# Optimization experiments

Measured on AMD Instinct MI355X. Metric: run time of the kernel, lower is better.

## Reference

```python
import jax, jax.numpy as jnp
import numpy as np

D_MODEL = 1024
NUM_HEADS = 16
D_K = D_MODEL // NUM_HEADS


def setup_inputs() -> dict:
    key = jax.random.key(0)
    ks = jax.random.split(key, 11)
    B, S = 4, 2048
    s = 1.0 / np.sqrt(D_MODEL)
    return {
        "query": jax.random.normal(ks[0], (B, S, D_MODEL), jnp.float32),
        "key": jax.random.normal(ks[1], (B, S, D_MODEL), jnp.float32),
        "value": jax.random.normal(ks[2], (B, S, D_MODEL), jnp.float32),
        "Wq": jax.random.normal(ks[3], (D_MODEL, D_MODEL), jnp.float32) * s,
        "bq": jnp.zeros((D_MODEL,), jnp.float32),
        "Wk": jax.random.normal(ks[4], (D_MODEL, D_MODEL), jnp.float32) * s,
        "bk": jnp.zeros((D_MODEL,), jnp.float32),
        "Wv": jax.random.normal(ks[5], (D_MODEL, D_MODEL), jnp.float32) * s,
        "bv": jnp.zeros((D_MODEL,), jnp.float32),
        "Wo": jax.random.normal(ks[6], (D_MODEL, D_MODEL), jnp.float32) * s,
        "bo": jnp.zeros((D_MODEL,), jnp.float32),
    }


def reference(query, key, value, Wq, bq, Wk, bk, Wv, bv, Wo, bo):
    B, Sq, _ = query.shape
    Sk = key.shape[1]
    # linear projections (torch Linear: x @ W.T + b)
    q = query @ Wq.T + bq
    k = key @ Wk.T + bk
    v = value @ Wv.T + bv
    # [B, H, S, d_k]
    q = q.reshape(B, Sq, NUM_HEADS, D_K).transpose(0, 2, 1, 3)
    k = k.reshape(B, Sk, NUM_HEADS, D_K).transpose(0, 2, 1, 3)
    v = v.reshape(B, Sk, NUM_HEADS, D_K).transpose(0, 2, 1, 3)
    scores = jnp.einsum("bhqd,bhkd->bhqk", q, k) / jnp.sqrt(jnp.float32(D_K)).astype(q.dtype)
    attn = jax.nn.softmax(scores, axis=-1)
    out = jnp.einsum("bhqk,bhkd->bhqd", attn, v)
    out = out.transpose(0, 2, 1, 3).reshape(B, Sq, D_MODEL)
    return out @ Wo.T + bo
```

## Files before the change

### kernel.cpp

```cpp
#include <hip/hip_runtime.h>
#include <hip/hip_bf16.h>
#include <cstdint>
#include <cstddef>

typedef __attribute__((ext_vector_type(8))) short bf16x8;
typedef __attribute__((ext_vector_type(4))) short bf16x4;
typedef __attribute__((ext_vector_type(4))) float f32x4;
typedef __attribute__((ext_vector_type(2))) unsigned int u32x2;

#define NH 16
#define DK 64
#define SEQ 2048
#define DM 1024
#define QSCALE 0.18033688011112042f

__device__ __forceinline__ short f2bf(float f) {
    union { float f; unsigned u; } x; x.f = f;
    unsigned r = x.u + 0x7fffu + ((x.u >> 16) & 1u);
    return (short)(r >> 16);
}

__device__ __forceinline__ unsigned pk2(float a, float b) {
    union { float f; unsigned u; } x, y; x.f = a; y.f = b;
    return __builtin_amdgcn_perm(y.u + 0x8000u, x.u + 0x8000u, 0x07060302u);
}

__device__ __forceinline__ void glds16(const short* g, short* l) {
    __builtin_amdgcn_global_load_lds((const __attribute__((address_space(1))) unsigned int*)g,
                                     (__attribute__((address_space(3))) unsigned int*)l, 16, 0, 0);
}

__global__ __launch_bounds__(256)
void cvt_x(const float* __restrict__ src, short* __restrict__ dst)
{
    int i = (blockIdx.x * 256 + threadIdx.x) * 8;
    float4 a = *(const float4*)&src[i];
    float4 b = *(const float4*)&src[i + 4];
    bf16x8 o = { f2bf(a.x), f2bf(a.y), f2bf(a.z), f2bf(a.w),
                 f2bf(b.x), f2bf(b.y), f2bf(b.z), f2bf(b.w) };
    *(bf16x8*)&dst[i] = o;
}

__global__ __launch_bounds__(256)
void cvt_w(const float* __restrict__ Wq, const float* __restrict__ Wk,
           const float* __restrict__ Wv, const float* __restrict__ Wo,
           short* __restrict__ dst)
{
    int z = blockIdx.y;
    const float* s = (z == 0) ? Wq : (z == 1) ? Wk : (z == 2) ? Wv : Wo;
    float sc = (z == 0) ? QSCALE : 1.0f;
    int i = (blockIdx.x * 256 + threadIdx.x) * 8;
    float4 a = *(const float4*)&s[i];
    float4 b = *(const float4*)&s[i + 4];
    bf16x8 o = { f2bf(a.x * sc), f2bf(a.y * sc), f2bf(a.z * sc), f2bf(a.w * sc),
                 f2bf(b.x * sc), f2bf(b.y * sc), f2bf(b.z * sc), f2bf(b.w * sc) };
    *(bf16x8*)&dst[(size_t)z * DM * DM + i] = o;
}

#define GEMM_CORE(P0, OFF0, P1, OFF1)                                                      \
    __shared__ short As[128 * 32];                                                         \
    __shared__ short Bs[128 * 32];                                                         \
    f32x4 acc[4][4] = {};                                                                  \
    const int t = threadIdx.x;                                                             \
    const int lane = t & 63;                                                               \
    const int w = t >> 6;                                                                  \
    const int wm = (w >> 1) * 64, wn = (w & 1) * 64;                                       \
    const int l15 = lane & 15, quad = lane >> 4;                                           \
    const int g0 = t, g1 = 256 + t;                                                        \
    const int r0 = g0 >> 2, r1 = g1 >> 2;                                                  \
    const int c0 = ((g0 & 3) ^ ((r0 >> 1) & 3)) * 8;                                       \
    const int c1 = ((g1 & 3) ^ ((r1 >> 1) & 3)) * 8;                                       \
    for (int k0 = 0; k0 < DM; k0 += 32) {                                                  \
        glds16(&P0[(size_t)(OFF0 + r0) * DM + k0 + c0], &As[g0 * 8]);                      \
        glds16(&P0[(size_t)(OFF0 + r1) * DM + k0 + c1], &As[g1 * 8]);                      \
        glds16(&P1[(size_t)(OFF1 + r0) * DM + k0 + c0], &Bs[g0 * 8]);                      \
        glds16(&P1[(size_t)(OFF1 + r1) * DM + k0 + c1], &Bs[g1 * 8]);                      \
        __syncthreads();                                                                   \
        bf16x8 a[4], b[4];                                                                 \
        _Pragma("unroll")                                                                  \
        for (int i = 0; i < 4; i++) {                                                      \
            int row = wm + i * 16 + l15;                                                   \
            a[i] = *(bf16x8*)&As[row * 32 + (quad ^ ((row >> 1) & 3)) * 8];                \
        }                                                                                  \
        _Pragma("unroll")                                                                  \
        for (int j = 0; j < 4; j++) {                                                      \
            int row = wn + j * 16 + l15;                                                   \
            b[j] = *(bf16x8*)&Bs[row * 32 + (quad ^ ((row >> 1) & 3)) * 8];                \
        }                                                                                  \
        _Pragma("unroll")                                                                  \
        for (int i = 0; i < 4; i++)                                                        \
            _Pragma("unroll")                                                              \
            for (int j = 0; j < 4; j++)                                                    \
                acc[i][j] = __builtin_amdgcn_mfma_f32_16x16x32_bf16(a[i], b[j], acc[i][j], 0, 0, 0); \
        __syncthreads();                                                                   \
    }

__global__ __launch_bounds__(256)
void gemm_qk(const short* __restrict__ X, const short* __restrict__ W,
             const float* __restrict__ bias, short* __restrict__ dst, float bscale)
{
    const int tn = blockIdx.x * 128;
    const int tm = blockIdx.y * 128;
    GEMM_CORE(W, tn, X, tm)

#pragma unroll
    for (int i = 0; i < 4; i++) {
        int n0 = tn + wm + i * 16 + quad * 4;
        float4 b4 = *(const float4*)&bias[n0];
        int h = n0 >> 6, d0 = n0 & 63;
#pragma unroll
        for (int j = 0; j < 4; j++) {
            int m = tm + wn + j * 16 + l15;
            int bb = m >> 11, s = m & (SEQ - 1);
            u32x2 u = { pk2(acc[i][j][0] + b4.x * bscale, acc[i][j][1] + b4.y * bscale),
                        pk2(acc[i][j][2] + b4.z * bscale, acc[i][j][3] + b4.w * bscale) };
            *(u32x2*)&dst[((((size_t)(bb * NH + h)) * SEQ + s) << 6) + d0] = u;
        }
    }
}

__global__ __launch_bounds__(256)
void gemm_v(const short* __restrict__ X, const short* __restrict__ W,
            const float* __restrict__ bias, short* __restrict__ dst)
{
    const int tn = blockIdx.x * 128;
    const int tm = blockIdx.y * 128;
    GEMM_CORE(X, tm, W, tn)

#pragma unroll
    for (int j = 0; j < 4; j++) {
        int n = tn + wn + j * 16 + l15;
        float bn = bias[n];
        int h = n >> 6, d = n & 63;
#pragma unroll
        for (int i = 0; i < 4; i++) {
            int m0 = tm + wm + i * 16 + quad * 4;
            int bb = m0 >> 11, s0 = m0 & (SEQ - 1);
            u32x2 u = { pk2(acc[i][j][0] + bn, acc[i][j][1] + bn),
                        pk2(acc[i][j][2] + bn, acc[i][j][3] + bn) };
            *(u32x2*)&dst[((size_t)((bb * NH + h) * 64 + d)) * SEQ + s0] = u;
        }
    }
}

__global__ __launch_bounds__(256)
void out_proj(const short* __restrict__ A, const short* __restrict__ W,
              const float* __restrict__ bias, float* __restrict__ out)
{
    const int tn = blockIdx.x * 128;
    const int tm = blockIdx.y * 128;
    GEMM_CORE(A, tm, W, tn)

#pragma unroll
    for (int j = 0; j < 4; j++) {
        int n = tn + wn + j * 16 + l15;
        float bn = bias[n];
#pragma unroll
        for (int i = 0; i < 4; i++)
#pragma unroll
            for (int r = 0; r < 4; r++) {
                int m = tm + wm + i * 16 + quad * 4 + r;
                out[(size_t)m * DM + n] = acc[i][j][r] + bn;
            }
    }
}

__global__ __launch_bounds__(256, 4)
void attn(const short* __restrict__ Q, const short* __restrict__ K, const short* __restrict__ V,
          short* __restrict__ O)
{
    const int bh = blockIdx.x;
    const int b = bh >> 4, h = bh & 15;
    const int qt = blockIdx.y;
    const size_t base = (size_t)bh * SEQ * DK;
    const size_t vbase = (size_t)bh * DK * SEQ;

    const int t = threadIdx.x;
    const int lane = t & 63;
    const int w = t >> 6;
    const int l15 = lane & 15, quad = lane >> 4;
    const int l7 = l15 & 7;

    __shared__ short Kt[64 * 64];
    __shared__ short Vt[64 * 64];
    __shared__ short Pt[4][32 * 64];

    bf16x8 qb[2][2];
    const int qrow0 = qt * 128 + w * 32;
#pragma unroll
    for (int nq = 0; nq < 2; nq++)
#pragma unroll
        for (int kd = 0; kd < 2; kd++)
            qb[nq][kd] = *(const bf16x8*)&Q[base + (size_t)(qrow0 + nq * 16 + l15) * DK + kd * 32 + quad * 8];

    f32x4 oT[4][2] = {};
    float l_[2] = { 0.0f, 0.0f };

    const int sr = t >> 2;
    const int sc = (t & 3) * 16;
    const int sg0 = (((t & 3) * 2) ^ (sr & 7)) * 8;
    const int sg1 = (((t & 3) * 2 + 1) ^ (sr & 7)) * 8;

    bf16x8 kr0 = *(const bf16x8*)&K[base + (size_t)sr * DK + sc];
    bf16x8 kr1 = *(const bf16x8*)&K[base + (size_t)sr * DK + sc + 8];
    bf16x8 vr0 = *(const bf16x8*)&V[vbase + (size_t)sr * SEQ + sc];
    bf16x8 vr1 = *(const bf16x8*)&V[vbase + (size_t)sr * SEQ + sc + 8];

    for (int kt = 0; kt < SEQ / 64; kt++) {
        *(bf16x8*)&Kt[sr * 64 + sg0] = kr0;
        *(bf16x8*)&Kt[sr * 64 + sg1] = kr1;
        *(bf16x8*)&Vt[sr * 64 + sg0] = vr0;
        *(bf16x8*)&Vt[sr * 64 + sg1] = vr1;
        __syncthreads();

        if (kt < SEQ / 64 - 1) {
            const short* kg = &K[base + (size_t)((kt + 1) * 64 + sr) * DK + sc];
            const short* vg = &V[vbase + (size_t)sr * SEQ + (kt + 1) * 64 + sc];
            kr0 = *(const bf16x8*)&kg[0];
            kr1 = *(const bf16x8*)&kg[8];
            vr0 = *(const bf16x8*)&vg[0];
            vr1 = *(const bf16x8*)&vg[8];
        }

        f32x4 st[4][2] = {};
#pragma unroll
        for (int kd = 0; kd < 2; kd++) {
#pragma unroll
            for (int mf = 0; mf < 4; mf++) {
                bf16x8 ka = *(bf16x8*)&Kt[(mf * 16 + l15) * 64 + ((kd * 4 + quad) ^ l7) * 8];
#pragma unroll
                for (int nq = 0; nq < 2; nq++)
                    st[mf][nq] = __builtin_amdgcn_mfma_f32_16x16x32_bf16(ka, qb[nq][kd], st[mf][nq], 0, 0, 0);
            }
        }

#pragma unroll
        for (int nq = 0; nq < 2; nq++) {
            float pm[4];
#pragma unroll
            for (int mf = 0; mf < 4; mf++) {
#pragma unroll
                for (int r = 0; r < 4; r++)
                    st[mf][nq][r] = __builtin_amdgcn_exp2f(st[mf][nq][r]);
                pm[mf] = (st[mf][nq][0] + st[mf][nq][1]) + (st[mf][nq][2] + st[mf][nq][3]);
            }
            float rs = (pm[0] + pm[1]) + (pm[2] + pm[3]);
            rs += __shfl_xor(rs, 16);
            rs += __shfl_xor(rs, 32);
            l_[nq] += rs;
            const int prow = (nq * 16 + l15) * 64;
#pragma unroll
            for (int mf = 0; mf < 4; mf++) {
                u32x2 u = { pk2(st[mf][nq][0], st[mf][nq][1]),
                            pk2(st[mf][nq][2], st[mf][nq][3]) };
                *(u32x2*)&Pt[w][prow + (((mf * 2 + (quad >> 1)) ^ l7) * 8) + (quad & 1) * 4] = u;
            }
        }

#pragma unroll
        for (int kk = 0; kk < 2; kk++) {
            bf16x8 pb[2];
#pragma unroll
            for (int nq = 0; nq < 2; nq++)
                pb[nq] = *(bf16x8*)&Pt[w][(nq * 16 + l15) * 64 + ((kk * 4 + quad) ^ l7) * 8];
#pragma unroll
            for (int mfd = 0; mfd < 4; mfd++) {
                bf16x8 va = *(bf16x8*)&Vt[(mfd * 16 + l15) * 64 + ((kk * 4 + quad) ^ l7) * 8];
#pragma unroll
                for (int nq = 0; nq < 2; nq++)
                    oT[mfd][nq] = __builtin_amdgcn_mfma_f32_16x16x32_bf16(va, pb[nq], oT[mfd][nq], 0, 0, 0);
            }
        }
        __syncthreads();
    }

#pragma unroll
    for (int nq = 0; nq < 2; nq++) {
        float inv = 1.0f / l_[nq];
        int s = qrow0 + nq * 16 + l15;
#pragma unroll
        for (int mfd = 0; mfd < 4; mfd++) {
            u32x2 u = { pk2(oT[mfd][nq][0] * inv, oT[mfd][nq][1] * inv),
                        pk2(oT[mfd][nq][2] * inv, oT[mfd][nq][3] * inv) };
            *(u32x2*)&O[((size_t)(b * SEQ + s)) * DM + h * 64 + mfd * 16 + quad * 4] = u;
        }
    }
}

extern "C" void kernel_launch(void* const* d_in, const int* in_sizes, int n_in,
                              void* d_out, int out_size, void* d_ws, size_t ws_size,
                              hipStream_t stream)
{
    const float* q_in = (const float*)d_in[0];
    const float* k_in = (const float*)d_in[1];
    const float* v_in = (const float*)d_in[2];
    const float* Wq = (const float*)d_in[3];
    const float* bq = (const float*)d_in[4];
    const float* Wk = (const float*)d_in[5];
    const float* bk = (const float*)d_in[6];
    const float* Wv = (const float*)d_in[7];
    const float* bv = (const float*)d_in[8];
    const float* Wo = (const float*)d_in[9];
    const float* bo = (const float*)d_in[10];
    float* out = (float*)d_out;

    char* ws = (char*)d_ws;
    const size_t MB = (size_t)1024 * 1024;
    short* xb  = (short*)(ws);
    short* vws = (short*)(ws + 16 * MB);
    short* ows = (short*)(ws + 32 * MB);
    short* Wb  = (short*)(ws + 48 * MB);
    short* qws = (short*)d_out;
    short* kws = (short*)d_out + (size_t)8 * MB;

    const size_t NW = (size_t)DM * DM;
    const int wblocks = (int)(NW / 2048);
    const int xblocks = (4 * SEQ * DM) / 2048;

    cvt_w<<<dim3(wblocks, 4), 256, 0, stream>>>(Wq, Wk, Wv, Wo, Wb);

    cvt_x<<<dim3(xblocks, 1), 256, 0, stream>>>(q_in, xb);
    gemm_qk<<<dim3(8, 64), 256, 0, stream>>>(xb, Wb + 0 * NW, bq, qws, QSCALE);
    cvt_x<<<dim3(xblocks, 1), 256, 0, stream>>>(k_in, xb);
    gemm_qk<<<dim3(8, 64), 256, 0, stream>>>(xb, Wb + 1 * NW, bk, kws, 1.0f);
    cvt_x<<<dim3(xblocks, 1), 256, 0, stream>>>(v_in, xb);
    gemm_v<<<dim3(8, 64), 256, 0, stream>>>(xb, Wb + 2 * NW, bv, vws);

    attn<<<dim3(64, 16), 256, 0, stream>>>(qws, kws, vws, ows);
    out_proj<<<dim3(8, 64), 256, 0, stream>>>(ows, Wb + 3 * NW, bo, out);
}
```

Before: 370.6 us.

## Batch QKV conversion and projection launches; fold softmax row-sum into PV MFMA

```diff
diff --git a/kernel.cpp b/kernel.cpp
--- a/kernel.cpp
+++ b/kernel.cpp
@@ -28,6 +28,38 @@
 __device__ __forceinline__ void glds16(const short* g, short* l) {
     __builtin_amdgcn_global_load_lds((const __attribute__((address_space(1))) unsigned int*)g,
                                      (__attribute__((address_space(3))) unsigned int*)l, 16, 0, 0);
+}
+
+__global__ __launch_bounds__(256)
+void cvt_all(const float* __restrict__ xq, const float* __restrict__ xk, const float* __restrict__ xv,
+             const float* __restrict__ Wq, const float* __restrict__ Wk,
+             const float* __restrict__ Wv, const float* __restrict__ Wo,
+             short* __restrict__ xb0, short* __restrict__ xb1, short* __restrict__ xb2,
+             short* __restrict__ Wb)
+{
+    const int bid = blockIdx.x;
+    const float* src;
+    short* dst;
+    float sc = 1.0f;
+    int i;
+    if (bid < 12288) {
+        int z = bid >> 12;
+        src = (z == 0) ? xq : (z == 1) ? xk : xv;
+        dst = (z == 0) ? xb0 : (z == 1) ? xb1 : xb2;
+        i = (bid & 4095) * 2048 + threadIdx.x * 8;
+    } else {
+        int wb = bid - 12288;
+        int z = wb >> 9;
+        src = (z == 0) ? Wq : (z == 1) ? Wk : (z == 2) ? Wv : Wo;
+        dst = Wb + (size_t)z * DM * DM;
+        sc = (z == 0) ? QSCALE : 1.0f;
+        i = (wb & 511) * 2048 + threadIdx.x * 8;
+    }
+    float4 a = *(const float4*)&src[i];
+    float4 b = *(const float4*)&src[i + 4];
+    bf16x8 o = { f2bf(a.x * sc), f2bf(a.y * sc), f2bf(a.z * sc), f2bf(a.w * sc),
+                 f2bf(b.x * sc), f2bf(b.y * sc), f2bf(b.z * sc), f2bf(b.w * sc) };
+    *(bf16x8*)&dst[i] = o;
 }
 
 __global__ __launch_bounds__(256)
@@ -96,49 +128,56 @@
     }
 
 __global__ __launch_bounds__(256)
-void gemm_qk(const short* __restrict__ X, const short* __restrict__ W,
-             const float* __restrict__ bias, short* __restrict__ dst, float bscale)
-{
+void gemm_qkv(const short* __restrict__ x0, const short* __restrict__ x1, const short* __restrict__ x2,
+              const short* __restrict__ Wball,
+              const float* __restrict__ bq, const float* __restrict__ bk, const float* __restrict__ bv,
+              short* __restrict__ qws, short* __restrict__ kws, short* __restrict__ vws,
+              int zoff)
+{
+    const int z = blockIdx.z + zoff;
+    const short* X = (z == 0) ? x0 : (z == 1) ? x1 : x2;
+    const short* W = Wball + (size_t)z * DM * DM;
+    const float* bias = (z == 0) ? bq : (z == 1) ? bk : bv;
+    const float bscale = (z == 0) ? QSCALE : 1.0f;
+
     const int tn = blockIdx.x * 128;
     const int tm = blockIdx.y * 128;
-    GEMM_CORE(W, tn, X, tm)
-
-#pragma unroll
-    for (int i = 0; i < 4; i++) {
-        int n0 = tn + wm + i * 16 + quad * 4;
-        float4 b4 = *(const float4*)&bias[n0];
-        int h = n0 >> 6, d0 = n0 & 63;
+    const int vm = (z == 2);
+
+    const short* P0 = vm ? X : W;   const int OFF0 = vm ? tm : tn;
+    const short* P1 = vm ? W : X;   const int OFF1 = vm ? tn : tm;
+    GEMM_CORE(P0, OFF0, P1, OFF1)
+
+    if (vm) {
 #pragma unroll
         for (int j = 0; j < 4; j++) {
-            int m = tm + wn + j * 16 + l15;
-            int bb = m >> 11, s = m & (SEQ - 1);
-            u32x2 u = { pk2(acc[i][j][0] + b4.x * bscale, acc[i][j][1] + b4.y * bscale),
-                        pk2(acc[i][j][2] + b4.z * bscale, acc[i][j][3] + b4.w * bscale) };
-            *(u32x2*)&dst[((((size_t)(bb * NH + h)) * SEQ + s) << 6) + d0] = u;
-        }
-    }
-}
-
-__global__ __launch_bounds__(256)
-void gemm_v(const short* __restrict__ X, const short* __restrict__ W,
-            const float* __restrict__ bias, short* __restrict__ dst)
-{
-    const int tn = blockIdx.x * 128;
-    const int tm = blockIdx.y * 128;
-    GEMM_CORE(X, tm, W, tn)
-
-#pragma unroll
-    for (int j = 0; j < 4; j++) {
-        int n = tn + wn + j * 16 + l15;
-        float bn = bias[n];
-        int h = n >> 6, d = n & 63;
+            int n = tn + wn + j * 16 + l15;
+            float bn = bias[n];
+            int h = n >> 6, d = n & 63;
+#pragma unroll
+            for (int i = 0; i < 4; i++) {
+                int m0 = tm + wm + i * 16 + quad * 4;
+                int bb = m0 >> 11, s0 = m0 & (SEQ - 1);
+                u32x2 u = { pk2(acc[i][j][0] + bn, acc[i][j][1] + bn),
+                            pk2(acc[i][j][2] + bn, acc[i][j][3] + bn) };
+                *(u32x2*)&vws[((size_t)((bb * NH + h) * 64 + d)) * SEQ + s0] = u;
+            }
+        }
+    } else {
+        short* dst = (z == 0) ? qws : kws;
 #pragma unroll
         for (int i = 0; i < 4; i++) {
-            int m0 = tm + wm + i * 16 + quad * 4;
-            int bb = m0 >> 11, s0 = m0 & (SEQ - 1);
-            u32x2 u = { pk2(acc[i][j][0] + bn, acc[i][j][1] + bn),
-                        pk2(acc[i][j][2] + bn, acc[i][j][3] + bn) };
-            *(u32x2*)&dst[((size_t)((bb * NH + h) * 64 + d)) * SEQ + s0] = u;
+            int n0 = tn + wm + i * 16 + quad * 4;
+            float4 b4 = *(const float4*)&bias[n0];
+            int h = n0 >> 6, d0 = n0 & 63;
+#pragma unroll
+            for (int j = 0; j < 4; j++) {
+                int m = tm + wn + j * 16 + l15;
+                int bb = m >> 11, s = m & (SEQ - 1);
+                u32x2 u = { pk2(acc[i][j][0] + b4.x * bscale, acc[i][j][1] + b4.y * bscale),
+                            pk2(acc[i][j][2] + b4.z * bscale, acc[i][j][3] + b4.w * bscale) };
+                *(u32x2*)&dst[((((size_t)(bb * NH + h)) * SEQ + s) << 6) + d0] = u;
+            }
         }
     }
 }
@@ -182,8 +221,15 @@
     const int l7 = l15 & 7;
 
     __shared__ short Kt[64 * 64];
-    __shared__ short Vt[64 * 64];
+    __shared__ short Vt[80 * 64];
     __shared__ short Pt[4][32 * 64];
+
+    if (t < 128) {
+        int row = 64 + (t >> 3);
+        short val = (row == 64) ? (short)0x3F80 : (short)0;
+        bf16x8 fill = { val, val, val, val, val, val, val, val };
+        *(bf16x8*)&Vt[row * 64 + (t & 7) * 8] = fill;
+    }
 
     bf16x8 qb[2][2];
     const int qrow0 = qt * 128 + w * 32;
@@ -193,8 +239,7 @@
         for (int kd = 0; kd < 2; kd++)
             qb[nq][kd] = *(const bf16x8*)&Q[base + (size_t)(qrow0 + nq * 16 + l15) * DK + kd * 32 + quad * 8];
 
-    f32x4 oT[4][2] = {};
-    float l_[2] = { 0.0f, 0.0f };
+    f32x4 oT[5][2] = {};
 
     const int sr = t >> 2;
     const int sc = (t & 3) * 16;
@@ -236,21 +281,12 @@
 
 #pragma unroll
         for (int nq = 0; nq < 2; nq++) {
-            float pm[4];
+            const int prow = (nq * 16 + l15) * 64;
 #pragma unroll
             for (int mf = 0; mf < 4; mf++) {
 #pragma unroll
                 for (int r = 0; r < 4; r++)
                     st[mf][nq][r] = __builtin_amdgcn_exp2f(st[mf][nq][r]);
-                pm[mf] = (st[mf][nq][0] + st[mf][nq][1]) + (st[mf][nq][2] + st[mf][nq][3]);
-            }
-            float rs = (pm[0] + pm[1]) + (pm[2] + pm[3]);
-            rs += __shfl_xor(rs, 16);
-            rs += __shfl_xor(rs, 32);
-            l_[nq] += rs;
-            const int prow = (nq * 16 + l15) * 64;
-#pragma unroll
-            for (int mf = 0; mf < 4; mf++) {
                 u32x2 u = { pk2(st[mf][nq][0], st[mf][nq][1]),
                             pk2(st[mf][nq][2], st[mf][nq][3]) };
                 *(u32x2*)&Pt[w][prow + (((mf * 2 + (quad >> 1)) ^ l7) * 8) + (quad & 1) * 4] = u;
@@ -264,7 +300,7 @@
             for (int nq = 0; nq < 2; nq++)
                 pb[nq] = *(bf16x8*)&Pt[w][(nq * 16 + l15) * 64 + ((kk * 4 + quad) ^ l7) * 8];
 #pragma unroll
-            for (int mfd = 0; mfd < 4; mfd++) {
+            for (int mfd = 0; mfd < 5; mfd++) {
                 bf16x8 va = *(bf16x8*)&Vt[(mfd * 16 + l15) * 64 + ((kk * 4 + quad) ^ l7) * 8];
 #pragma unroll
                 for (int nq = 0; nq < 2; nq++)
@@ -276,7 +312,8 @@
 
 #pragma unroll
     for (int nq = 0; nq < 2; nq++) {
-        float inv = 1.0f / l_[nq];
+        float lsum = __shfl(oT[4][nq][0], l15);
+        float inv = 1.0f / lsum;
         int s = qrow0 + nq * 16 + l15;
 #pragma unroll
         for (int mfd = 0; mfd < 4; mfd++) {
@@ -306,26 +343,37 @@
 
     char* ws = (char*)d_ws;
     const size_t MB = (size_t)1024 * 1024;
-    short* xb  = (short*)(ws);
-    short* vws = (short*)(ws + 16 * MB);
-    short* ows = (short*)(ws + 32 * MB);
-    short* Wb  = (short*)(ws + 48 * MB);
     short* qws = (short*)d_out;
     short* kws = (short*)d_out + (size_t)8 * MB;
-
     const size_t NW = (size_t)DM * DM;
-    const int wblocks = (int)(NW / 2048);
-    const int xblocks = (4 * SEQ * DM) / 2048;
-
-    cvt_w<<<dim3(wblocks, 4), 256, 0, stream>>>(Wq, Wk, Wv, Wo, Wb);
-
-    cvt_x<<<dim3(xblocks, 1), 256, 0, stream>>>(q_in, xb);
-    gemm_qk<<<dim3(8, 64), 256, 0, stream>>>(xb, Wb + 0 * NW, bq, qws, QSCALE);
-    cvt_x<<<dim3(xblocks, 1), 256, 0, stream>>>(k_in, xb);
-    gemm_qk<<<dim3(8, 64), 256, 0, stream>>>(xb, Wb + 1 * NW, bk, kws, 1.0f);
-    cvt_x<<<dim3(xblocks, 1), 256, 0, stream>>>(v_in, xb);
-    gemm_v<<<dim3(8, 64), 256, 0, stream>>>(xb, Wb + 2 * NW, bv, vws);
-
-    attn<<<dim3(64, 16), 256, 0, stream>>>(qws, kws, vws, ows);
-    out_proj<<<dim3(8, 64), 256, 0, stream>>>(ows, Wb + 3 * NW, bo, out);
-}
+
+    if (ws_size >= 88 * MB) {
+        short* xb0 = (short*)(ws);
+        short* xb1 = (short*)(ws + 16 * MB);
+        short* xb2 = (short*)(ws + 32 * MB);
+        short* vws = (short*)(ws + 48 * MB);
+        short* ows = (short*)(ws + 64 * MB);
+        short* Wb  = (short*)(ws + 80 * MB);
+
+        cvt_all<<<dim3(14336), 256, 0, stream>>>(q_in, k_in, v_in, Wq, Wk, Wv, Wo, xb0, xb1, xb2, Wb);
+        gemm_qkv<<<dim3(8, 64, 3), 256, 0, stream>>>(xb0, xb1, xb2, Wb, bq, bk, bv, qws, kws, vws, 0);
+        attn<<<dim3(64, 16), 256, 0, stream>>>(qws, kws, vws, ows);
+        out_proj<<<dim3(8, 64), 256, 0, stream>>>(ows, Wb + 3 * NW, bo, out);
+    } else {
+        short* xb  = (short*)(ws);
+        short* vws = (short*)(ws + 16 * MB);
+        short* ows = (short*)(ws + 32 * MB);
+        short* Wb  = (short*)(ws + 48 * MB);
+        const int xblocks = (4 * SEQ * DM) / 2048;
+
+        cvt_w<<<dim3((int)(NW / 2048), 4), 256, 0, stream>>>(Wq, Wk, Wv, Wo, Wb);
+        cvt_x<<<dim3(xblocks), 256, 0, stream>>>(q_in, xb);
+        gemm_qkv<<<dim3(8, 64, 1), 256, 0, stream>>>(xb, xb, xb, Wb, bq, bk, bv, qws, kws, vws, 0);
+        cvt_x<<<dim3(xblocks), 256, 0, stream>>>(k_in, xb);
+        gemm_qkv<<<dim3(8, 64, 1), 256, 0, stream>>>(xb, xb, xb, Wb, bq, bk, bv, qws, kws, vws, 1);
+        cvt_x<<<dim3(xblocks), 256, 0, stream>>>(v_in, xb);
+        gemm_qkv<<<dim3(8, 64, 1), 256, 0, stream>>>(xb, xb, xb, Wb, bq, bk, bv, qws, kws, vws, 2);
+        attn<<<dim3(64, 16), 256, 0, stream>>>(qws, kws, vws, ows);
+        out_proj<<<dim3(8, 64), 256, 0, stream>>>(ows, Wb + 3 * NW, bo, out);
+    }
+}
```

Result: faster. 349.0 us (-5.8%).
